# Performance work log

Measured on AMD Instinct MI355X. Metric: run time of the kernel, lower is better.

Reference implementation:

```python
import jax, jax.numpy as jnp
import numpy as np

B, IMG, P, NP, S = 16, 224, 16, 196, 197
D, H, DH, L, FF = 768, 12, 64, 12, 3072


def setup_inputs() -> dict:
    key = jax.random.key(0)
    ks = jax.random.split(key, 16)
    nrm = lambda k, shape: jax.random.normal(k, shape, jnp.float32) * 0.02
    return {
        "x": jax.random.normal(ks[0], (B, IMG, IMG, 3), jnp.float32),
        "cls": jnp.zeros((1, 1, D), jnp.float32),
        "pos_emb": nrm(ks[1], (S, D)),
        "Wp": nrm(ks[2], (P * P * 3, D)), "bp": jnp.zeros((D,), jnp.float32),
        "Wq": nrm(ks[3], (L, D, D)), "bq": jnp.zeros((L, D), jnp.float32),
        "Wk": nrm(ks[4], (L, D, D)), "bk": jnp.zeros((L, D), jnp.float32),
        "Wv": nrm(ks[5], (L, D, D)), "bv": jnp.zeros((L, D), jnp.float32),
        "Wo": nrm(ks[6], (L, D, D)), "bo": jnp.zeros((L, D), jnp.float32),
        "ln1g": jnp.ones((L, D), jnp.float32), "ln1b": jnp.zeros((L, D), jnp.float32),
        "ln2g": jnp.ones((L, D), jnp.float32), "ln2b": jnp.zeros((L, D), jnp.float32),
        "W1": nrm(ks[7], (L, D, FF)), "b1": jnp.zeros((L, FF), jnp.float32),
        "W2": nrm(ks[8], (L, FF, D)), "b2": jnp.zeros((L, D), jnp.float32),
        "lnfg": jnp.ones((D,), jnp.float32), "lnfb": jnp.zeros((D,), jnp.float32),
    }


def _ln(y, g, b, eps):
    m = y.mean(-1, keepdims=True)
    v = ((y - m) ** 2).mean(-1, keepdims=True)
    return (y - m) / jnp.sqrt(v + eps) * g + b


def _gelu(z):
    # tanh-approx GeLU, exactly as in the source module
    return 0.5 * z * (1.0 + jnp.tanh(np.sqrt(2.0 / np.pi) * (z + 0.044715 * z ** 3)))


def reference(x, cls, pos_emb, Wp, bp, Wq, bq, Wk, bk, Wv, bv, Wo, bo,
              ln1g, ln1b, ln2g, ln2b, W1, b1, W2, b2, lnfg, lnfb):
    Bb = x.shape[0]
    g = IMG // P  # 14 patches per side
    # tf.image.extract_patches with VALID, stride==size: row-major patch flatten
    patches = x.reshape(Bb, g, P, g, P, 3).transpose(0, 1, 3, 2, 4, 5).reshape(Bb, NP, P * P * 3)
    h = patches @ Wp + bp                               # [B, 196, D]
    h = jnp.concatenate([jnp.broadcast_to(cls, (Bb, 1, D)), h], axis=1) + pos_emb  # [B, S, D]

    scale = np.float32(1.0 / np.sqrt(DH))

    def block(h, p):
        wq, bq_, wk, bk_, wv, bv_, wo, bo_, g1, gb1, g2, gb2, w1, b1_, w2, b2_ = p
        y = _ln(h, g1, gb1, 1e-6)
        q = (y @ wq + bq_).reshape(Bb, S, H, DH).transpose(0, 2, 1, 3)  # [B,H,S,dh]
        k = (y @ wk + bk_).reshape(Bb, S, H, DH).transpose(0, 2, 1, 3)
        v = (y @ wv + bv_).reshape(Bb, S, H, DH).transpose(0, 2, 1, 3)
        w = jax.nn.softmax(jnp.einsum('bhqd,bhkd->bhqk', q, k) * scale, axis=-1)
        att = jnp.einsum('bhqk,bhkd->bhqd', w, v)       # [B,H,S,dh]
        # NOTE: in the source the two Permutes cancel, so the "concat" is a raw
        # reshape of the [B,H,S,dh] tensor to [B,S,D] (heads interleaved). Faithful.
        concat = att.reshape(Bb, S, D)
        h1 = h + concat @ wo + bo_
        y = _ln(h1, g2, gb2, 1e-6)
        y = _gelu(y @ w1 + b1_) @ w2 + b2_
        return h1 + y, None

    h, _ = jax.lax.scan(block, h, (Wq, bq, Wk, bk, Wv, bv, Wo, bo,
                                   ln1g, ln1b, ln2g, ln2b, W1, b1, W2, b2))
    return _ln(h, lnfg, lnfb, 1e-3)  # final Keras LayerNorm, default eps=1e-3
```

## Files before the change

### kernel.cpp

```cpp
#include <hip/hip_runtime.h>
#include <cstdint>
#include <cstddef>

#define DD   768
#define HHN  12
#define SS   197
#define FFD  3072
#define MROWS 3152
#define MPAD  3200
#define PROWS 3136

typedef __attribute__((ext_vector_type(4))) float  f32x4;
typedef __attribute__((ext_vector_type(8))) __bf16 bf16x8;
typedef __attribute__((ext_vector_type(4))) __bf16 bf16x4;

__global__ __launch_bounds__(256) void w2b_k(const float* __restrict__ W, __bf16* __restrict__ Wb, int N)
{
  __shared__ float Ws[64][65];
  const int t = threadIdx.x;
  const int n0 = blockIdx.x * 64, k0 = blockIdx.y * 64;
  const int nl = t & 63, kq = t >> 6;
  #pragma unroll
  for (int i = 0; i < 16; ++i) {
    const int k = kq * 16 + i;
    Ws[k][nl] = W[(size_t)(k0 + k) * N + n0 + nl];
  }
  __syncthreads();
  #pragma unroll
  for (int r = 0; r < 2; ++r) {
    const int c = r * 256 + t;
    const int kh = c >> 6, n = c & 63;
    bf16x8 v;
    #pragma unroll
    for (int j = 0; j < 8; ++j) v[j] = (__bf16)Ws[kh * 8 + j][n];
    *(bf16x8*)(Wb + ((size_t)((k0 >> 3) + kh) * N + n0 + n) * 8) = v;
  }
}

template<int BN, int NMAT, int MODE, bool GELU_, bool STOREBF>
__global__ __launch_bounds__(256) void gemm_k(
    const __bf16* __restrict__ A,
    const __bf16* __restrict__ Bb0, const __bf16* __restrict__ Bb1, const __bf16* __restrict__ Bb2,
    const float* __restrict__ bias0, const float* __restrict__ bias1, const float* __restrict__ bias2,
    float* __restrict__ Cf, __bf16* __restrict__ Cb,
    int N, int Kloc, int Kstride)
{
  constexpr int BUFB = (BN == 128) ? 16384 : 12288;
  __shared__ char lds[3 * BUFB];
  const int tid = threadIdx.x;
  const int m0 = blockIdx.y * 128;
  const int n0 = blockIdx.x * BN;
  const int kz = blockIdx.z;
  const size_t kOff = (size_t)kz * Kloc;

  int mat = 0, nB = n0, NBw = N;
  const __bf16* Bbp = Bb0; const float* biasp = bias0;
  if (NMAT == 3) {
    mat = n0 / DD; nB = n0 - mat * DD; NBw = DD;
    Bbp   = (mat == 0) ? Bb0   : ((mat == 1) ? Bb1   : Bb2);
    biasp = (mat == 0) ? bias0 : ((mat == 1) ? bias1 : bias2);
  }

  constexpr int NC = (BN == 128) ? 4 : 2;
  f32x4 acc[4][NC];
  const f32x4 z4 = {0.f, 0.f, 0.f, 0.f};
  #pragma unroll
  for (int i = 0; i < 4; ++i)
    #pragma unroll
    for (int j = 0; j < NC; ++j) acc[i][j] = z4;

  const int lane = tid & 63;
  const int wv = tid >> 6;
  const int wr = wv >> 1, wc = wv & 1;
  const int arow = tid & 127, akh = tid >> 7;

  const int nKB = Kloc >> 5;

  auto issue = [&](int kt, int buf) {
    const int k0 = kt << 5;
    char* Ab = lds + buf * BUFB;
    char* Bb = Ab + 8192;
    {
      const __bf16* ga0 = A + (size_t)(m0 + arow) * Kstride + kOff + k0 + akh * 8;
      auto g0 = (__attribute__((address_space(1))) unsigned int*)(uintptr_t)ga0;
      auto g1 = (__attribute__((address_space(1))) unsigned int*)(uintptr_t)(ga0 + 16);
      auto l0 = (__attribute__((address_space(3))) unsigned int*)(uintptr_t)(Ab + wv * 1024);
      auto l1 = (__attribute__((address_space(3))) unsigned int*)(uintptr_t)(Ab + 4096 + wv * 1024);
      __builtin_amdgcn_global_load_lds(g0, l0, 16, 0, 0);
      __builtin_amdgcn_global_load_lds(g1, l1, 16, 0, 0);
    }
    if (BN == 128) {
      #pragma unroll
      for (int r = 0; r < 2; ++r) {
        const int c = r * 256 + tid;
        const int g = c >> 7, col = c & 127;
        const __bf16* gb = Bbp + ((size_t)(((kOff + k0) >> 3) + g) * NBw + nB + col) * 8;
        auto gp = (__attribute__((address_space(1))) unsigned int*)(uintptr_t)gb;
        auto lp = (__attribute__((address_space(3))) unsigned int*)(uintptr_t)(Bb + r * 4096 + wv * 1024);
        __builtin_amdgcn_global_load_lds(gp, lp, 16, 0, 0);
      }
    } else {
      const __bf16* gb = Bbp + ((size_t)(((kOff + k0) >> 3) + wv) * NBw + nB + lane) * 8;
      auto gp = (__attribute__((address_space(1))) unsigned int*)(uintptr_t)gb;
      auto lp = (__attribute__((address_space(3))) unsigned int*)(uintptr_t)(Bb + wv * 1024);
      __builtin_amdgcn_global_load_lds(gp, lp, 16, 0, 0);
    }
  };

  constexpr int WAITIMM = (BN == 128) ? 0xF78  : 0xF76 ;

  issue(0, 0);
  issue(nKB > 1 ? 1 : 0, 1);

  int cb = 0, wb = 2;
  const int q = lane >> 4, r16 = lane & 15;
  for (int kb = 0; kb < nKB; ++kb) {
    __builtin_amdgcn_sched_barrier(0);
    __builtin_amdgcn_s_barrier();
    const int nxt = kb + 2;
    issue(nxt < nKB ? nxt : nKB - 1, wb);
    __builtin_amdgcn_s_waitcnt(WAITIMM);
    __builtin_amdgcn_s_barrier();
    __builtin_amdgcn_sched_barrier(0);

    const char* Ab = lds + cb * BUFB;
    const char* Bb = Ab + 8192;
    const char* pa = Ab + q * 2048 + (wr * 64 + r16) * 16;
    const char* pb = (BN == 128) ? (Bb + q * 2048 + (wc * 64 + r16) * 16)
                                 : (Bb + q * 1024 + (wc * 32 + r16) * 16);
    bf16x8 af[4], bfv[NC];
    #pragma unroll
    for (int i = 0; i < 4; ++i) af[i]  = *(const bf16x8*)(pa + i * 256);
    #pragma unroll
    for (int i = 0; i < NC; ++i) bfv[i] = *(const bf16x8*)(pb + i * 256);
    #pragma unroll
    for (int ri = 0; ri < 4; ++ri)
      #pragma unroll
      for (int ci = 0; ci < NC; ++ci)
        acc[ri][ci] = __builtin_amdgcn_mfma_f32_16x16x32_bf16(af[ri], bfv[ci], acc[ri][ci], 0, 0, 0);

    cb = (cb == 2) ? 0 : cb + 1;
    wb = (wb == 2) ? 0 : wb + 1;
  }
  __builtin_amdgcn_s_waitcnt(0);

  const int q4 = (lane >> 4) * 4, c16 = lane & 15;
  #pragma unroll
  for (int ci = 0; ci < NC; ++ci) {
    const int n = n0 + ((BN == 128) ? wc * 64 : wc * 32) + ci * 16 + c16;
    const float bsv = (MODE == 1 && kz != 0) ? 0.f
                      : biasp[(NMAT == 3) ? (n - mat * DD) : n];
    #pragma unroll
    for (int ri = 0; ri < 4; ++ri) {
      const int mb = m0 + wr * 64 + ri * 16 + q4;
      #pragma unroll
      for (int rg = 0; rg < 4; ++rg) {
        float v = acc[ri][ci][rg] + bsv;
        const size_t off = (size_t)(mb + rg) * N + n;
        if (MODE == 1) {
          atomicAdd(&Cf[off], v);
        } else {
          if (GELU_) {
            const float zz = v;
            const float a = 0.7978845608028654f * (zz + 0.044715f * zz * zz * zz);
            v = 0.5f * zz * (2.0f - 2.0f / (1.0f + __expf(2.0f * a)));
          }
          if (STOREBF) Cb[off] = (__bf16)v; else Cf[off] = v;
        }
      }
    }
  }
}

__global__ __launch_bounds__(256) void attn_k(const __bf16* __restrict__ qkv, __bf16* __restrict__ att)
{
  __shared__ char als[58240];
  const int t = threadIdx.x;
  const int qt = blockIdx.x, bh = blockIdx.y;
  const int b = bh / HHN, hh = bh % HHN;
  const int r0 = qt * 64;

  #pragma unroll
  for (int i = 0; i < 7; ++i) {
    const int c = t + i * 256;
    const int kh = c & 7, s = c >> 3;
    const int sg = s < SS ? s : (SS - 1);
    const bf16x8 v = *(const bf16x8*)(qkv + (size_t)(b * SS + sg) * 2304 + DD + hh * 64 + kh * 8);
    *(bf16x8*)(als + kh * 3600 + s * 16) = v;
  }
  #pragma unroll
  for (int i = 0; i < 2; ++i) {
    const int c = t + i * 256;
    const int qr = c & 63, dh8 = c >> 6;
    const int rr = r0 + qr;
    const int sg = rr < SS ? rr : (SS - 1);
    const bf16x8 v = *(const bf16x8*)(qkv + (size_t)(b * SS + sg) * 2304 + hh * 64 + dh8 * 8);
    *(bf16x8*)(als + 28800 + dh8 * 1040 + qr * 16) = v;
  }
  __syncthreads();

  const int w = t >> 6, lane = t & 63;
  const int q = lane >> 4, c16 = lane & 15;
  const f32x4 z4 = {0.f, 0.f, 0.f, 0.f};

  f32x4 acc[13];
  #pragma unroll
  for (int nt = 0; nt < 13; ++nt) acc[nt] = z4;
  #pragma unroll
  for (int kk = 0; kk < 2; ++kk) {
    const bf16x8 af = *(const bf16x8*)(als + 28800 + (kk * 4 + q) * 1040 + (w * 16 + c16) * 16);
    #pragma unroll
    for (int nt = 0; nt < 13; ++nt) {
      const bf16x8 bf_ = *(const bf16x8*)(als + (kk * 4 + q) * 3600 + (nt * 16 + c16) * 16);
      acc[nt] = __builtin_amdgcn_mfma_f32_16x16x32_bf16(af, bf_, acc[nt], 0, 0, 0);
    }
  }
  __syncthreads();

  float inv[4];
  #pragma unroll
  for (int rg = 0; rg < 4; ++rg) {
    float mx = -1e30f;
    #pragma unroll
    for (int nt = 0; nt < 13; ++nt) {
      const bool val = (nt < 12) || (c16 < 5);
      const float sv = acc[nt][rg] * 0.125f;
      if (val) mx = fmaxf(mx, sv);
    }
    #pragma unroll
    for (int m = 1; m < 16; m <<= 1) mx = fmaxf(mx, __shfl_xor(mx, m, 16));
    float sm = 0.f;
    #pragma unroll
    for (int nt = 0; nt < 13; ++nt) {
      const bool val = (nt < 12) || (c16 < 5);
      const float e = val ? __expf(acc[nt][rg] * 0.125f - mx) : 0.f;
      acc[nt][rg] = e; sm += e;
    }
    #pragma unroll
    for (int m = 1; m < 16; m <<= 1) sm += __shfl_xor(sm, m, 16);
    inv[rg] = 1.f / sm;
  }

  #pragma unroll
  for (int nt = 0; nt < 14; ++nt) {
    #pragma unroll
    for (int rg = 0; rg < 4; ++rg) {
      const int s = nt * 16 + c16;
      const int qr = w * 16 + q * 4 + rg;
      const float pv = (nt < 13) ? acc[nt][rg] * inv[rg] : 0.f;
      *(__bf16*)(als + (s >> 3) * 1040 + qr * 16 + (s & 7) * 2) = (__bf16)pv;
    }
  }
  if (t < 224) {
    const int sg = t < SS ? t : (SS - 1);
    const __bf16* vrow = qkv + (size_t)(b * SS + sg) * 2304 + 1536 + hh * 64;
    #pragma unroll
    for (int dh8 = 0; dh8 < 8; ++dh8) {
      const bf16x8 v = *(const bf16x8*)(vrow + dh8 * 8);
      #pragma unroll
      for (int j = 0; j < 8; ++j)
        *(__bf16*)(als + 29120 + (t >> 3) * 1040 + (dh8 * 8 + j) * 16 + (t & 7) * 2) = v[j];
    }
  }
  __syncthreads();

  f32x4 o[4];
  #pragma unroll
  for (int dt = 0; dt < 4; ++dt) o[dt] = z4;
  #pragma unroll
  for (int kk = 0; kk < 7; ++kk) {
    const bf16x8 af = *(const bf16x8*)(als + (kk * 4 + q) * 1040 + (w * 16 + c16) * 16);
    #pragma unroll
    for (int dt = 0; dt < 4; ++dt) {
      const bf16x8 bf_ = *(const bf16x8*)(als + 29120 + (kk * 4 + q) * 1040 + (dt * 16 + c16) * 16);
      o[dt] = __builtin_amdgcn_mfma_f32_16x16x32_bf16(af, bf_, o[dt], 0, 0, 0);
    }
  }
  #pragma unroll
  for (int dt = 0; dt < 4; ++dt) {
    #pragma unroll
    for (int rg = 0; rg < 4; ++rg) {
      const int r = r0 + w * 16 + q * 4 + rg;
      if (r < SS)
        att[((size_t)bh * SS + r) * 64 + dt * 16 + c16] = (__bf16)o[dt][rg];
    }
  }
}

template<bool OUTBF>
__global__ __launch_bounds__(256) void ln_k(const float* __restrict__ X,
    const float* __restrict__ g, const float* __restrict__ be, float eps,
    __bf16* __restrict__ Yb, float* __restrict__ Yf)
{
  const int row = blockIdx.x * 4 + (threadIdx.x >> 6), l = threadIdx.x & 63;
  const f32x4* xr = (const f32x4*)(X + (size_t)row * DD);
  f32x4 v[3];
  #pragma unroll
  for (int j = 0; j < 3; ++j) v[j] = xr[l + j * 64];
  float s = 0.f;
  #pragma unroll
  for (int j = 0; j < 3; ++j) s += v[j][0] + v[j][1] + v[j][2] + v[j][3];
  #pragma unroll
  for (int m = 1; m < 64; m <<= 1) s += __shfl_xor(s, m, 64);
  const float mean = s * (1.f / 768.f);
  float vs = 0.f;
  #pragma unroll
  for (int j = 0; j < 3; ++j)
    #pragma unroll
    for (int e = 0; e < 4; ++e) { const float d = v[j][e] - mean; vs += d * d; }
  #pragma unroll
  for (int m = 1; m < 64; m <<= 1) vs += __shfl_xor(vs, m, 64);
  const float rstd = rsqrtf(vs * (1.f / 768.f) + eps);
  const f32x4* gp = (const f32x4*)g; const f32x4* bp = (const f32x4*)be;
  #pragma unroll
  for (int j = 0; j < 3; ++j) {
    const int c4 = l + j * 64;
    const f32x4 gg = gp[c4], bb = bp[c4];
    if (OUTBF) {
      bf16x4 o;
      #pragma unroll
      for (int e = 0; e < 4; ++e) o[e] = (__bf16)((v[j][e] - mean) * rstd * gg[e] + bb[e]);
      *(bf16x4*)(Yb + (size_t)row * DD + c4 * 4) = o;
    } else {
      f32x4 o;
      #pragma unroll
      for (int e = 0; e < 4; ++e) o[e] = (v[j][e] - mean) * rstd * gg[e] + bb[e];
      *(f32x4*)(Yf + (size_t)row * DD + c4 * 4) = o;
    }
  }
}

__global__ __launch_bounds__(256) void im2col_k(const float* __restrict__ x, __bf16* __restrict__ patches)
{
  const int idx = blockIdx.x * 256 + threadIdx.x;
  const int row = idx / 768, col = idx % 768;
  float v = 0.f;
  if (row < PROWS) {
    const int b = row / 196, p = row % 196;
    const int py = p / 14, px = p % 14;
    const int r = col / 48, rem = col % 48, c = rem / 3, ch = rem % 3;
    v = x[((size_t)(b * 224 + py * 16 + r) * 224 + (px * 16 + c)) * 3 + ch];
  }
  patches[idx] = (__bf16)v;
}

__global__ __launch_bounds__(256) void assemble_k(const float* __restrict__ tmp, const float* __restrict__ cls,
    const float* __restrict__ pos, float* __restrict__ h)
{
  const int idx = blockIdx.x * 256 + threadIdx.x;
  const int row = idx / 192, qc = (idx % 192) * 4;
  f32x4 v = {0.f, 0.f, 0.f, 0.f};
  if (row < MROWS) {
    const int b = row / SS, s2 = row % SS;
    if (s2 == 0) v = *(const f32x4*)(cls + qc);
    else         v = *(const f32x4*)(tmp + (size_t)(b * 196 + s2 - 1) * 768 + qc);
    const f32x4 p = *(const f32x4*)(pos + (size_t)s2 * 768 + qc);
    v += p;
  }
  *(f32x4*)(h + (size_t)row * 768 + qc) = v;
}

extern "C" void kernel_launch(void* const* d_in, const int* in_sizes, int n_in,
                              void* d_out, int out_size, void* d_ws, size_t ws_size,
                              hipStream_t stream)
{
  (void)in_sizes; (void)n_in; (void)out_size;
  const float* x    = (const float*)d_in[0];
  const float* cls  = (const float*)d_in[1];
  const float* pos  = (const float*)d_in[2];
  const float* Wp   = (const float*)d_in[3];
  const float* bp   = (const float*)d_in[4];
  const float* Wq   = (const float*)d_in[5];
  const float* bq   = (const float*)d_in[6];
  const float* Wk   = (const float*)d_in[7];
  const float* bk   = (const float*)d_in[8];
  const float* Wv   = (const float*)d_in[9];
  const float* bv   = (const float*)d_in[10];
  const float* Wo   = (const float*)d_in[11];
  const float* bo   = (const float*)d_in[12];
  const float* ln1g = (const float*)d_in[13];
  const float* ln1b = (const float*)d_in[14];
  const float* ln2g = (const float*)d_in[15];
  const float* ln2b = (const float*)d_in[16];
  const float* W1   = (const float*)d_in[17];
  const float* b1   = (const float*)d_in[18];
  const float* W2   = (const float*)d_in[19];
  const float* b2   = (const float*)d_in[20];
  const float* lnfg = (const float*)d_in[21];
  const float* lnfb = (const float*)d_in[22];

  char* ws = (char*)d_ws;
  float*  h    = (float*) (ws + 0);
  __bf16* y    = (__bf16*)(ws + 9830400);
  __bf16* qkv  = (__bf16*)(ws + 14745600);
  float*  tmp  = (float*) (ws + 14745600);
  __bf16* att  = (__bf16*)(ws + 29491200);
  __bf16* mffn = (__bf16*)(ws + 34406400);
  __bf16* patches = (__bf16*)(ws + 34406400);
  __bf16* Wpb = (__bf16*)(ws + 54067200);
  __bf16* Wqb = (__bf16*)(ws + 55246848);
  __bf16* Wkb = (__bf16*)(ws + 69402624);
  __bf16* Wvb = (__bf16*)(ws + 83558400);
  __bf16* Wob = (__bf16*)(ws + 97714176);
  __bf16* W1b = (__bf16*)(ws + 111869952);
  __bf16* W2b = (__bf16*)(ws + 168493056);
  if (ws_size < 225116160) return;

  w2b_k<<<dim3(12, 12),  256, 0, stream>>>(Wp, Wpb, DD);
  w2b_k<<<dim3(12, 144), 256, 0, stream>>>(Wq, Wqb, DD);
  w2b_k<<<dim3(12, 144), 256, 0, stream>>>(Wk, Wkb, DD);
  w2b_k<<<dim3(12, 144), 256, 0, stream>>>(Wv, Wvb, DD);
  w2b_k<<<dim3(12, 144), 256, 0, stream>>>(Wo, Wob, DD);
  w2b_k<<<dim3(48, 144), 256, 0, stream>>>(W1, W1b, FFD);
  w2b_k<<<dim3(12, 576), 256, 0, stream>>>(W2, W2b, DD);

  im2col_k<<<MPAD * 768 / 256, 256, 0, stream>>>(x, patches);
  gemm_k<64,1,0,false,false><<<dim3(12,25), 256, 0, stream>>>(
      patches, Wpb,Wpb,Wpb, bp,bp,bp, tmp, nullptr, DD, DD, DD);
  assemble_k<<<MPAD * 192 / 256, 256, 0, stream>>>(tmp, cls, pos, h);

  for (int l = 0; l < 12; ++l) {
    const size_t wDD = (size_t)l * DD * DD, wFF = (size_t)l * DD * FFD;
    ln_k<true><<<MROWS / 4, 256, 0, stream>>>(h, ln1g + l*DD, ln1b + l*DD, 1e-6f, y, nullptr);
    gemm_k<64,3,0,false,true><<<dim3(36,25), 256, 0, stream>>>(
        y, Wqb + wDD, Wkb + wDD, Wvb + wDD,
        bq + l*DD, bk + l*DD, bv + l*DD, nullptr, qkv, 3*DD, DD, DD);
    attn_k<<<dim3(4, 192), 256, 0, stream>>>(qkv, att);
    gemm_k<64,1,1,false,false><<<dim3(12,25), 256, 0, stream>>>(
        att, Wob + wDD, nullptr, nullptr, bo + l*DD, nullptr, nullptr,
        h, nullptr, DD, DD, DD);
    ln_k<true><<<MROWS / 4, 256, 0, stream>>>(h, ln2g + l*DD, ln2b + l*DD, 1e-6f, y, nullptr);
    gemm_k<128,1,0,true,true><<<dim3(24,25), 256, 0, stream>>>(
        y, W1b + wFF, nullptr, nullptr, b1 + l*FFD, nullptr, nullptr,
        nullptr, mffn, FFD, DD, DD);
    gemm_k<64,1,1,false,false><<<dim3(12,25,2), 256, 0, stream>>>(
        mffn, W2b + wFF, nullptr, nullptr, b2 + l*DD, nullptr, nullptr,
        h, nullptr, DD, FFD/2, FFD);
  }
  ln_k<false><<<MROWS / 4, 256, 0, stream>>>(h, lnfg, lnfb, 1e-3f, nullptr, (float*)d_out);
}
```

Before: 2.522 ms.

## Write V transposed from QKV GEMM epilogue and remap GEMM grid tiles

The QKV GEMM epilogue now writes the V third straight into a per-(batch,head) transposed buffer. The attention kernel can then load V with vectorized contiguous reads instead of scalar transposing stores into LDS. GEMM launches also switch to a 1D grid with M-tiles grouped per N column, meant to improve B-tile cache reuse across blocks, at the cost of idle padded blocks. The QKV and W2 GEMMs move to 128-wide N tiles. The V epilogue uses scattered 2-byte stores, which may be poorly coalesced.

```diff
diff --git a/kernel.cpp b/kernel.cpp
--- a/kernel.cpp
+++ b/kernel.cpp
@@ -37,21 +37,24 @@
   }
 }
 
-template<int BN, int NMAT, int MODE, bool GELU_, bool STOREBF>
+template<int BN, int NMAT, int MODE, bool GELU_, bool STOREBF, bool VT>
 __global__ __launch_bounds__(256) void gemm_k(
     const __bf16* __restrict__ A,
     const __bf16* __restrict__ Bb0, const __bf16* __restrict__ Bb1, const __bf16* __restrict__ Bb2,
     const float* __restrict__ bias0, const float* __restrict__ bias1, const float* __restrict__ bias2,
-    float* __restrict__ Cf, __bf16* __restrict__ Cb,
+    float* __restrict__ Cf, __bf16* __restrict__ Cb, __bf16* __restrict__ vt,
     int N, int Kloc, int Kstride)
 {
+  const int mt = blockIdx.x & 31;
+  if (mt >= 25) return;
+  const int m0 = mt * 128;
+  const int n0 = (blockIdx.x >> 5) * BN;
+  const int kz = blockIdx.y;
+  const size_t kOff = (size_t)kz * Kloc;
+
   constexpr int BUFB = (BN == 128) ? 16384 : 12288;
   __shared__ char lds[3 * BUFB];
   const int tid = threadIdx.x;
-  const int m0 = blockIdx.y * 128;
-  const int n0 = blockIdx.x * BN;
-  const int kz = blockIdx.z;
-  const size_t kOff = (size_t)kz * Kloc;
 
   int mat = 0, nB = n0, NBw = N;
   const __bf16* Bbp = Bb0; const float* biasp = bias0;
@@ -79,7 +82,7 @@
   auto issue = [&](int kt, int buf) {
     const int k0 = kt << 5;
     char* Ab = lds + buf * BUFB;
-    char* Bb = Ab + 8192;
+    char* Bbl = Ab + 8192;
     {
       const __bf16* ga0 = A + (size_t)(m0 + arow) * Kstride + kOff + k0 + akh * 8;
       auto g0 = (__attribute__((address_space(1))) unsigned int*)(uintptr_t)ga0;
@@ -96,13 +99,13 @@
         const int g = c >> 7, col = c & 127;
         const __bf16* gb = Bbp + ((size_t)(((kOff + k0) >> 3) + g) * NBw + nB + col) * 8;
         auto gp = (__attribute__((address_space(1))) unsigned int*)(uintptr_t)gb;
-        auto lp = (__attribute__((address_space(3))) unsigned int*)(uintptr_t)(Bb + r * 4096 + wv * 1024);
+        auto lp = (__attribute__((address_space(3))) unsigned int*)(uintptr_t)(Bbl + r * 4096 + wv * 1024);
         __builtin_amdgcn_global_load_lds(gp, lp, 16, 0, 0);
       }
     } else {
       const __bf16* gb = Bbp + ((size_t)(((kOff + k0) >> 3) + wv) * NBw + nB + lane) * 8;
       auto gp = (__attribute__((address_space(1))) unsigned int*)(uintptr_t)gb;
-      auto lp = (__attribute__((address_space(3))) unsigned int*)(uintptr_t)(Bb + wv * 1024);
+      auto lp = (__attribute__((address_space(3))) unsigned int*)(uintptr_t)(Bbl + wv * 1024);
       __builtin_amdgcn_global_load_lds(gp, lp, 16, 0, 0);
     }
   };
@@ -124,10 +127,10 @@
     __builtin_amdgcn_sched_barrier(0);
 
     const char* Ab = lds + cb * BUFB;
-    const char* Bb = Ab + 8192;
+    const char* Bbl = Ab + 8192;
     const char* pa = Ab + q * 2048 + (wr * 64 + r16) * 16;
-    const char* pb = (BN == 128) ? (Bb + q * 2048 + (wc * 64 + r16) * 16)
-                                 : (Bb + q * 1024 + (wc * 32 + r16) * 16);
+    const char* pb = (BN == 128) ? (Bbl + q * 2048 + (wc * 64 + r16) * 16)
+                                 : (Bbl + q * 1024 + (wc * 32 + r16) * 16);
     bf16x8 af[4], bfv[NC];
     #pragma unroll
     for (int i = 0; i < 4; ++i) af[i]  = *(const bf16x8*)(pa + i * 256);
@@ -156,29 +159,47 @@
       #pragma unroll
       for (int rg = 0; rg < 4; ++rg) {
         float v = acc[ri][ci][rg] + bsv;
-        const size_t off = (size_t)(mb + rg) * N + n;
-        if (MODE == 1) {
-          atomicAdd(&Cf[off], v);
+        const int row = mb + rg;
+        if (VT && NMAT == 3 && mat == 2) {
+          const int b = row / SS;
+          if (b < 16) {
+            const int s = row - b * SS;
+            const int nloc = n - 2 * DD;
+            const int hh = nloc >> 6, d = nloc & 63;
+            vt[((size_t)(b * HHN + hh) * 28 + (s >> 3)) * 512 + d * 8 + (s & 7)] = (__bf16)v;
+          }
         } else {
-          if (GELU_) {
-            const float zz = v;
-            const float a = 0.7978845608028654f * (zz + 0.044715f * zz * zz * zz);
-            v = 0.5f * zz * (2.0f - 2.0f / (1.0f + __expf(2.0f * a)));
+          const size_t off = (size_t)row * N + n;
+          if (MODE == 1) {
+            atomicAdd(&Cf[off], v);
+          } else {
+            if (GELU_) {
+              const float zz = v;
+              const float a = 0.7978845608028654f * (zz + 0.044715f * zz * zz * zz);
+              v = 0.5f * zz * (2.0f - 2.0f / (1.0f + __expf(2.0f * a)));
+            }
+            if (STOREBF) Cb[off] = (__bf16)v; else Cf[off] = v;
           }
-          if (STOREBF) Cb[off] = (__bf16)v; else Cf[off] = v;
         }
       }
     }
   }
 }
 
-__global__ __launch_bounds__(256) void attn_k(const __bf16* __restrict__ qkv, __bf16* __restrict__ att)
+__global__ __launch_bounds__(256) void attn_k(const __bf16* __restrict__ qkv,
+                                              const __bf16* __restrict__ vt,
+                                              __bf16* __restrict__ att)
 {
   __shared__ char als[58240];
   const int t = threadIdx.x;
   const int qt = blockIdx.x, bh = blockIdx.y;
   const int b = bh / HHN, hh = bh % HHN;
   const int r0 = qt * 64;
+
+  bf16x8 vstage[7];
+  #pragma unroll
+  for (int i = 0; i < 7; ++i)
+    vstage[i] = *(const bf16x8*)(vt + (size_t)bh * 14336 + (size_t)(t + i * 256) * 8);
 
   #pragma unroll
   for (int i = 0; i < 7; ++i) {
@@ -251,16 +272,10 @@
       *(__bf16*)(als + (s >> 3) * 1040 + qr * 16 + (s & 7) * 2) = (__bf16)pv;
     }
   }
-  if (t < 224) {
-    const int sg = t < SS ? t : (SS - 1);
-    const __bf16* vrow = qkv + (size_t)(b * SS + sg) * 2304 + 1536 + hh * 64;
-    #pragma unroll
-    for (int dh8 = 0; dh8 < 8; ++dh8) {
-      const bf16x8 v = *(const bf16x8*)(vrow + dh8 * 8);
-      #pragma unroll
-      for (int j = 0; j < 8; ++j)
-        *(__bf16*)(als + 29120 + (t >> 3) * 1040 + (dh8 * 8 + j) * 16 + (t & 7) * 2) = v[j];
-    }
+  #pragma unroll
+  for (int i = 0; i < 7; ++i) {
+    const int c = t + i * 256;
+    *(bf16x8*)(als + 29120 + (c >> 6) * 1040 + (c & 63) * 16) = vstage[i];
   }
   __syncthreads();
 
@@ -404,7 +419,8 @@
   __bf16* Wob = (__bf16*)(ws + 97714176);
   __bf16* W1b = (__bf16*)(ws + 111869952);
   __bf16* W2b = (__bf16*)(ws + 168493056);
-  if (ws_size < 225116160) return;
+  __bf16* vt  = (__bf16*)(ws + 225116160);
+  if (ws_size < 230621184) return;
 
   w2b_k<<<dim3(12, 12),  256, 0, stream>>>(Wp, Wpb, DD);
   w2b_k<<<dim3(12, 144), 256, 0, stream>>>(Wq, Wqb, DD);
@@ -415,27 +431,27 @@
   w2b_k<<<dim3(12, 576), 256, 0, stream>>>(W2, W2b, DD);
 
   im2col_k<<<MPAD * 768 / 256, 256, 0, stream>>>(x, patches);
-  gemm_k<64,1,0,false,false><<<dim3(12,25), 256, 0, stream>>>(
-      patches, Wpb,Wpb,Wpb, bp,bp,bp, tmp, nullptr, DD, DD, DD);
+  gemm_k<64,1,0,false,false,false><<<12*32, 256, 0, stream>>>(
+      patches, Wpb,Wpb,Wpb, bp,bp,bp, tmp, nullptr, nullptr, DD, DD, DD);
   assemble_k<<<MPAD * 192 / 256, 256, 0, stream>>>(tmp, cls, pos, h);
 
   for (int l = 0; l < 12; ++l) {
     const size_t wDD = (size_t)l * DD * DD, wFF = (size_t)l * DD * FFD;
     ln_k<true><<<MROWS / 4, 256, 0, stream>>>(h, ln1g + l*DD, ln1b + l*DD, 1e-6f, y, nullptr);
-    gemm_k<64,3,0,false,true><<<dim3(36,25), 256, 0, stream>>>(
+    gemm_k<128,3,0,false,true,true><<<18*32, 256, 0, stream>>>(
         y, Wqb + wDD, Wkb + wDD, Wvb + wDD,
-        bq + l*DD, bk + l*DD, bv + l*DD, nullptr, qkv, 3*DD, DD, DD);
-    attn_k<<<dim3(4, 192), 256, 0, stream>>>(qkv, att);
-    gemm_k<64,1,1,false,false><<<dim3(12,25), 256, 0, stream>>>(
+        bq + l*DD, bk + l*DD, bv + l*DD, nullptr, qkv, vt, 3*DD, DD, DD);
+    attn_k<<<dim3(4, 192), 256, 0, stream>>>(qkv, vt, att);
+    gemm_k<64,1,1,false,false,false><<<12*32, 256, 0, stream>>>(
         att, Wob + wDD, nullptr, nullptr, bo + l*DD, nullptr, nullptr,
-        h, nullptr, DD, DD, DD);
+        h, nullptr, nullptr, DD, DD, DD);
     ln_k<true><<<MROWS / 4, 256, 0, stream>>>(h, ln2g + l*DD, ln2b + l*DD, 1e-6f, y, nullptr);
-    gemm_k<128,1,0,true,true><<<dim3(24,25), 256, 0, stream>>>(
+    gemm_k<128,1,0,true,true,false><<<24*32, 256, 0, stream>>>(
         y, W1b + wFF, nullptr, nullptr, b1 + l*FFD, nullptr, nullptr,
-        nullptr, mffn, FFD, DD, DD);
-    gemm_k<64,1,1,false,false><<<dim3(12,25,2), 256, 0, stream>>>(
+        nullptr, mffn, nullptr, FFD, DD, DD);
+    gemm_k<128,1,1,false,false,false><<<dim3(6*32, 2), 256, 0, stream>>>(
         mffn, W2b + wFF, nullptr, nullptr, b2 + l*DD, nullptr, nullptr,
-        h, nullptr, DD, FFD/2, FFD);
+        h, nullptr, nullptr, DD, FFD/2, FFD);
   }
   ln_k<false><<<MROWS / 4, 256, 0, stream>>>(h, lnfg, lnfb, 1e-3f, nullptr, (float*)d_out);
 }
```

New measurement: 2.430 ms. 3.6% less time.
